# Performance work log

Hardware: AMD Instinct MI355X
Metric: run time of the kernel (lower is better)

Reference implementation:

```python
import jax, jax.numpy as jnp
import numpy as np

V, H, L, NH, MAXS = 32000, 1024, 6, 16, 2048
HD = H // NH
FF = 4 * H
EPS = 1e-5


def _ln(x, s, b):
    m = jnp.mean(x, axis=-1, keepdims=True)
    v = jnp.mean(jnp.square(x - m), axis=-1, keepdims=True)
    return (x - m) * jax.lax.rsqrt(v + EPS) * s + b


def setup_inputs() -> dict:
    key = jax.random.key(0)
    ks = jax.random.split(key, 12)
    s = 0.02
    inp = {
        "input_ids": jax.random.randint(ks[0], (2, 1024), 0, V, dtype=jnp.int64),
        "token_emb": jax.random.normal(ks[1], (V, H), jnp.float32) * s,
        "pos_emb": jax.random.normal(ks[2], (MAXS, H), jnp.float32) * s,
        "ln1_s": jnp.ones((L, H), jnp.float32),
        "ln1_b": jnp.zeros((L, H), jnp.float32),
        "qkv_w": jax.random.normal(ks[3], (L, H, 3 * H), jnp.float32) * s,
        "qkv_b": jnp.zeros((L, 3 * H), jnp.float32),
        "out_w": jax.random.normal(ks[4], (L, H, H), jnp.float32) * s,
        "out_b": jnp.zeros((L, H), jnp.float32),
        "ln2_s": jnp.ones((L, H), jnp.float32),
        "ln2_b": jnp.zeros((L, H), jnp.float32),
        "w1": jax.random.normal(ks[5], (L, H, FF), jnp.float32) * s,
        "b1": jnp.zeros((L, FF), jnp.float32),
        "w2": jax.random.normal(ks[6], (L, FF, H), jnp.float32) * s,
        "b2": jnp.zeros((L, H), jnp.float32),
        "lnf_s": jnp.ones((H,), jnp.float32),
        "lnf_b": jnp.zeros((H,), jnp.float32),
        "lm_w": jax.random.normal(ks[7], (H, V), jnp.float32) * s,
    }
    return inp


def reference(input_ids, token_emb, pos_emb, ln1_s, ln1_b, qkv_w, qkv_b,
              out_w, out_b, ln2_s, ln2_b, w1, b1, w2, b2, lnf_s, lnf_b, lm_w):
    B, S = input_ids.shape
    x = token_emb[input_ids] + pos_emb[:S][None]  # [B,S,H]; dropout = identity (eval)
    for i in range(L):
        # --- attention block ---
        h = _ln(x, ln1_s[i], ln1_b[i])
        qkv = h @ qkv_w[i] + qkv_b[i]                      # [B,S,3H]
        q, k, v = jnp.split(qkv, 3, axis=-1)
        q = q.reshape(B, S, NH, HD)
        k = k.reshape(B, S, NH, HD)
        v = v.reshape(B, S, NH, HD)
        scores = jnp.einsum('bqhd,bkhd->bhqk', q, k) / jnp.sqrt(jnp.float32(HD))
        attn = jax.nn.softmax(scores, axis=-1)             # non-causal, as in source
        o = jnp.einsum('bhqk,bkhd->bqhd', attn, v).reshape(B, S, H)
        x = x + o @ out_w[i] + out_b[i]
        # --- mlp block ---
        h = _ln(x, ln2_s[i], ln2_b[i])
        h = jax.nn.gelu(h @ w1[i] + b1[i], approximate=False)
        x = x + h @ w2[i] + b2[i]
    x = _ln(x, lnf_s, lnf_b)
    logits = x @ lm_w                                      # [B,S,V]
    return logits
```

## Files before the change

### kernel.cpp

```cpp
#include <hip/hip_runtime.h>
#include <hip/hip_bf16.h>
#include <cstdint>
#include <cstddef>

typedef __bf16 bf16;
typedef __attribute__((ext_vector_type(8))) __bf16 bf16x8;
typedef __attribute__((ext_vector_type(4))) __bf16 bf16x4;
typedef __attribute__((ext_vector_type(4))) float f32x4;

__device__ __forceinline__ f32x4 mfma16(bf16x8 a, bf16x8 b, f32x4 c) {
    return __builtin_amdgcn_mfma_f32_16x16x32_bf16(a, b, c, 0, 0, 0);
}

__device__ __forceinline__ void async_copy16(const void* g, void* l) {
    __builtin_amdgcn_global_load_lds((const __attribute__((address_space(1))) void*)g,
                                     (__attribute__((address_space(3))) void*)l,
                                     16, 0, 0);
}

template<int Ncnt> __device__ __forceinline__ void waitv();
template<> __device__ __forceinline__ void waitv<0>() { asm volatile("s_waitcnt vmcnt(0)" ::: "memory"); }
template<> __device__ __forceinline__ void waitv<2>() { asm volatile("s_waitcnt vmcnt(2)" ::: "memory"); }
template<> __device__ __forceinline__ void waitv<3>() { asm volatile("s_waitcnt vmcnt(3)" ::: "memory"); }
template<> __device__ __forceinline__ void waitv<4>() { asm volatile("s_waitcnt vmcnt(4)" ::: "memory"); }

__global__ __launch_bounds__(256)
void embed_kernel(const int* __restrict__ ids, const float* __restrict__ te,
                  const float* __restrict__ pe, float* __restrict__ x)
{
    const int row = blockIdx.x;
    const int s = row & 1023;
    const int id = ids[row];
    const f32x4* a = (const f32x4*)(te + (size_t)id * 1024);
    const f32x4* b = (const f32x4*)(pe + (size_t)s * 1024);
    f32x4* o = (f32x4*)(x + (size_t)row * 1024);
    o[threadIdx.x] = a[threadIdx.x] + b[threadIdx.x];
}

__device__ __forceinline__ void ln_body(const float* __restrict__ x, const float* __restrict__ sc,
                                        const float* __restrict__ bi, bf16* __restrict__ out,
                                        int row, int t, float* red)
{
    const f32x4 v = ((const f32x4*)(x + (size_t)row * 1024))[t];
    float s = v[0] + v[1] + v[2] + v[3];
    float q = v[0]*v[0] + v[1]*v[1] + v[2]*v[2] + v[3]*v[3];
    #pragma unroll
    for (int o = 1; o < 64; o <<= 1) { s += __shfl_xor(s, o); q += __shfl_xor(q, o); }
    const int wv = t >> 6, lane = t & 63;
    if (lane == 0) { red[wv] = s; red[4 + wv] = q; }
    __syncthreads();
    s = red[0] + red[1] + red[2] + red[3];
    q = red[4] + red[5] + red[6] + red[7];
    const float mean = s * (1.f / 1024.f);
    const float var  = q * (1.f / 1024.f) - mean * mean;
    const float rstd = rsqrtf(var + 1e-5f);
    const f32x4 scv = ((const f32x4*)sc)[t];
    const f32x4 biv = ((const f32x4*)bi)[t];
    bf16x4 o4;
    #pragma unroll
    for (int j = 0; j < 4; j++) o4[j] = (bf16)((v[j] - mean) * rstd * scv[j] + biv[j]);
    *(bf16x4*)(out + (size_t)row * 1024 + t * 4) = o4;
}

__device__ __forceinline__ void wcvt_body(const float* __restrict__ W, bf16* __restrict__ BT,
                                          int K, int N, int bid, int tidx, float (*tile)[65])
{
    const int nx = N >> 6;
    const int n0 = (bid % nx) << 6, k0 = (bid / nx) << 6;
    const int tx = tidx & 15, ty = tidx >> 4;
    #pragma unroll
    for (int r = 0; r < 4; r++) {
        const f32x4 v = *(const f32x4*)&W[(size_t)(k0 + ty + r*16) * N + n0 + tx*4];
        tile[ty + r*16][tx*4 + 0] = v[0];
        tile[ty + r*16][tx*4 + 1] = v[1];
        tile[ty + r*16][tx*4 + 2] = v[2];
        tile[ty + r*16][tx*4 + 3] = v[3];
    }
    __syncthreads();
    #pragma unroll
    for (int r = 0; r < 4; r++) {
        const int n = ty + r*16;
        bf16x4 o;
        #pragma unroll
        for (int j = 0; j < 4; j++) o[j] = (bf16)tile[tx*4 + j][n];
        *(bf16x4*)&BT[(size_t)(n0 + n) * K + k0 + tx*4] = o;
    }
}

__global__ __launch_bounds__(256)
void fused_ln_wcvt(const float* __restrict__ x, const float* __restrict__ sc,
                   const float* __restrict__ bi, bf16* __restrict__ out,
                   const float* __restrict__ W1, bf16* __restrict__ BT1, int K1, int N1, int nb1,
                   const float* __restrict__ W2, bf16* __restrict__ BT2, int K2, int N2)
{
    __shared__ float tile[64][65];
    __shared__ float red[8];
    const int bid = blockIdx.x, t = threadIdx.x;
    if (bid < 2048) {
        ln_body(x, sc, bi, out, bid, t, red);
    } else {
        const int wb = bid - 2048;
        if (wb < nb1) wcvt_body(W1, BT1, K1, N1, wb, t, tile);
        else          wcvt_body(W2, BT2, K2, N2, wb - nb1, t, tile);
    }
}

__global__ __launch_bounds__(256)
void fused_attn_wcvt(const bf16* __restrict__ qkv, bf16* __restrict__ attno,
                     const float* __restrict__ W, bf16* __restrict__ BT, int K, int N)
{
    __shared__ __align__(16) bf16 Ksh[128 * 64];
    __shared__ __align__(16) bf16 Vt[64][136];
    __shared__ __align__(16) bf16 Plds[4][16][132];
    __shared__ float tile[64][65];

    const int bid = blockIdx.x, tid = threadIdx.x;
    if (bid >= 512) {
        wcvt_body(W, BT, K, N, bid - 512, tid, tile);
        return;
    }
    const int b = (bid & 31) >> 4, h = bid & 15;
    const int qb = bid >> 5;
    const int lane = tid & 63, wave = tid >> 6;
    const bf16* base = qkv + (size_t)b * 1024 * 3072;
    const int qrow0 = qb * 64 + wave * 16;
    const int l15 = lane & 15;

    bf16x8 aQ[2];
    {
        const int qr = qrow0 + l15;
        const bf16* qp = base + (size_t)qr * 3072 + h * 64 + ((lane >> 4) << 3);
        aQ[0] = *(const bf16x8*)qp;
        aQ[1] = *(const bf16x8*)(qp + 32);
    }
    float m_i[4] = {-1e30f, -1e30f, -1e30f, -1e30f};
    float l_i[4] = {0.f, 0.f, 0.f, 0.f};
    f32x4 acc[4];
    #pragma unroll
    for (int nb = 0; nb < 4; nb++) acc[nb] = f32x4{0.f, 0.f, 0.f, 0.f};

    const int swzA = (((lane >> 4)     ^ (lane & 7)) << 3);
    const int swzB = (((4 + (lane >> 4)) ^ (lane & 7)) << 3);

    for (int ck = 0; ck < 8; ck++) {
        __syncthreads();
        #pragma unroll
        for (int p = 0; p < 4; p++) {
            const int c = p * 256 + tid;
            const int rw = c >> 3;
            const int kc = (c & 7) ^ (rw & 7);
            async_copy16(base + (size_t)(ck*128 + rw) * 3072 + 1024 + h*64 + kc*8, &Ksh[c * 8]);
        }
        #pragma unroll
        for (int p = 0; p < 4; p++) {
            const int idx = p * 256 + tid;
            const int keyl = idx >> 3, dc = idx & 7;
            const bf16x8 v = *(const bf16x8*)&base[(size_t)(ck*128 + keyl) * 3072 + 2048 + h*64 + dc*8];
            #pragma unroll
            for (int e = 0; e < 8; e++) Vt[dc*8 + e][keyl] = v[e];
        }
        __syncthreads();

        f32x4 sc[8];
        #pragma unroll
        for (int kk = 0; kk < 4; kk++) {
            const int kr0 = (kk*32 + l15) * 64;
            const int kr1 = kr0 + 16*64;
            f32x4 z{0.f, 0.f, 0.f, 0.f};
            z = mfma16(aQ[0], *(const bf16x8*)&Ksh[kr0 + swzA], z);
            z = mfma16(aQ[1], *(const bf16x8*)&Ksh[kr0 + swzB], z);
            sc[2*kk] = z;
            f32x4 z2{0.f, 0.f, 0.f, 0.f};
            z2 = mfma16(aQ[0], *(const bf16x8*)&Ksh[kr1 + swzA], z2);
            z2 = mfma16(aQ[1], *(const bf16x8*)&Ksh[kr1 + swzB], z2);
            sc[2*kk+1] = z2;
        }

        float c[4];
        #pragma unroll
        for (int i = 0; i < 4; i++) {
            float t = sc[0][i];
            #pragma unroll
            for (int e = 1; e < 8; e++) t = fmaxf(t, sc[e][i]);
            #pragma unroll
            for (int o = 1; o < 16; o <<= 1) t = fmaxf(t, __shfl_xor(t, o));
            t *= 0.125f;
            const float mnew = fmaxf(m_i[i], t);
            c[i] = __expf(m_i[i] - mnew);
            float p[8];
            float rs = 0.f;
            #pragma unroll
            for (int e = 0; e < 8; e++) {
                p[e] = __expf(fmaf(sc[e][i], 0.125f, -mnew));
                rs += p[e];
            }
            #pragma unroll
            for (int o = 1; o < 16; o <<= 1) rs += __shfl_xor(rs, o);
            l_i[i] = l_i[i] * c[i] + rs;
            m_i[i] = mnew;
            const int pr = ((lane >> 4) << 2) + i;
            #pragma unroll
            for (int e = 0; e < 8; e++)
                Plds[wave][pr][(e >> 1) * 32 + (e & 1) * 16 + l15] = (bf16)p[e];
        }
        #pragma unroll
        for (int nb = 0; nb < 4; nb++) {
            f32x4 a = acc[nb];
            a[0] *= c[0]; a[1] *= c[1]; a[2] *= c[2]; a[3] *= c[3];
            acc[nb] = a;
        }

        #pragma unroll
        for (int kk = 0; kk < 4; kk++) {
            const bf16x8 aP = *(const bf16x8*)&Plds[wave][l15][kk*32 + ((lane >> 4) << 3)];
            #pragma unroll
            for (int nb = 0; nb < 4; nb++) {
                const bf16x8 bV = *(const bf16x8*)&Vt[nb*16 + l15][kk*32 + ((lane >> 4) << 3)];
                acc[nb] = mfma16(aP, bV, acc[nb]);
            }
        }
    }
    #pragma unroll
    for (int nb = 0; nb < 4; nb++) {
        #pragma unroll
        for (int i = 0; i < 4; i++) {
            const int row = qrow0 + ((lane >> 4) << 2) + i;
            const float o = acc[nb][i] / l_i[i];
            attno[(size_t)(b*1024 + row) * 1024 + h*64 + nb*16 + l15] = (bf16)o;
        }
    }
}

template<int BM, int BN, int EPI, int KSPLIT>
__global__ __launch_bounds__(256)
void gemm_kernel(const bf16* __restrict__ A, const bf16* __restrict__ BT,
                 const float* __restrict__ bias, float* __restrict__ resid,
                 bf16* __restrict__ outb, float* __restrict__ outf,
                 int N, int K)
{
    constexpr int MT = 2048 / BM;
    constexpr int WM = BM / 2, WN = BN / 2;
    constexpr int FM = WM / 16, FN = WN / 16;
    constexpr int CA = BM / 32, CB = BN / 32;
    __shared__ __align__(16) bf16 Asmem[BM * 64];
    __shared__ __align__(16) bf16 Bsmem[BN * 64];

    const int nwg = gridDim.x;
    const int q = nwg >> 3, rr = nwg & 7;
    const int xcd = blockIdx.x & 7, ix = blockIdx.x >> 3;
    const int nid = (xcd < rr ? xcd * (q + 1) : rr * (q + 1) + (xcd - rr) * q) + ix;
    const int tiles = nwg / KSPLIT;
    const int ks = nid / tiles;
    const int tile = nid % tiles;
    const int bm = tile % MT, bn = tile / MT;

    const int tid = threadIdx.x;
    const int lane = tid & 63, wave = tid >> 6;
    const int wr = wave >> 1, wc = wave & 1;
    f32x4 acc[FM][FN];
    #pragma unroll
    for (int m = 0; m < FM; m++)
        #pragma unroll
        for (int n = 0; n < FN; n++) acc[m][n] = f32x4{0.f, 0.f, 0.f, 0.f};

    const bf16* Abase = A  + (size_t)bm * BM * K;
    const bf16* Bbase = BT + (size_t)bn * BN * K;
    const int K64 = K >> 6;
    const int ktlo = ks * (K64 / KSPLIT), kthi = ktlo + (K64 / KSPLIT);
    for (int kt = ktlo; kt < kthi; kt++) {
        __syncthreads();
        #pragma unroll
        for (int p = 0; p < CA; p++) {
            const int idx = p * 256 + tid;
            const int r = idx >> 3, c = (idx & 7) << 3;
            async_copy16(Abase + (size_t)r * K + kt * 64 + c, Asmem + idx * 8);
        }
        #pragma unroll
        for (int p = 0; p < CB; p++) {
            const int idx = p * 256 + tid;
            const int r = idx >> 3, c = (idx & 7) << 3;
            async_copy16(Bbase + (size_t)r * K + kt * 64 + c, Bsmem + idx * 8);
        }
        __syncthreads();
        #pragma unroll
        for (int kss = 0; kss < 2; kss++) {
            bf16x8 af[FM], bfv[FN];
            const int ko = kss * 32 + ((lane >> 4) << 3);
            const int ar = wr * WM + (lane & 15);
            const int br = wc * WN + (lane & 15);
            #pragma unroll
            for (int m = 0; m < FM; m++) af[m]  = *(const bf16x8*)&Asmem[(ar + m*16) * 64 + ko];
            #pragma unroll
            for (int n = 0; n < FN; n++) bfv[n] = *(const bf16x8*)&Bsmem[(br + n*16) * 64 + ko];
            #pragma unroll
            for (int m = 0; m < FM; m++)
                #pragma unroll
                for (int n = 0; n < FN; n++)
                    acc[m][n] = mfma16(af[m], bfv[n], acc[m][n]);
        }
    }
    const int r0 = bm * BM + wr * WM + ((lane >> 4) << 2);
    const int c0 = bn * BN + wc * WN + (lane & 15);
    #pragma unroll
    for (int n = 0; n < FN; n++) {
        const int col = c0 + n * 16;
        const float bv = (EPI == 3) ? 0.f : ((KSPLIT > 1 && ks != 0) ? 0.f : bias[col]);
        #pragma unroll
        for (int m = 0; m < FM; m++) {
            const int row = r0 + m * 16;
            const f32x4 a = acc[m][n];
            #pragma unroll
            for (int i = 0; i < 4; i++) {
                const float v = a[i] + bv;
                const size_t off = (size_t)(row + i) * N + col;
                if constexpr (EPI == 0) outb[off] = (bf16)v;
                else if constexpr (EPI == 1) {
                    if constexpr (KSPLIT > 1) atomicAdd(&resid[off], v);
                    else resid[off] += v;
                }
                else if constexpr (EPI == 2) {
                    const float g = 0.5f * v * (1.f + erff(v * 0.70710678118f));
                    outb[off] = (bf16)g;
                } else outf[off] = v;
            }
        }
    }
}

template<int BM, int BN, int EPI, int KSPLIT>
__global__ __launch_bounds__(512, 2)
void gemm256_kernel(const bf16* __restrict__ A, const bf16* __restrict__ BT,
                    const float* __restrict__ bias, float* __restrict__ resid,
                    bf16* __restrict__ outb, float* __restrict__ outf,
                    int N, int K)
{
    constexpr int MT = 2048 / BM;
    constexpr int FM = BM / 32;
    constexpr int FN = BN / 64;
    constexpr int HM = FM / 2;
    constexpr int LA = BM / 128, LB = BN / 128;
    constexpr int ASUB = BM * 32;
    constexpr int BSUB = BN * 32;
    extern __shared__ __align__(16) char smem_raw[];
    bf16* smem = (bf16*)smem_raw;

    const int nwg = gridDim.x;
    const int q = nwg >> 3, rr = nwg & 7;
    const int xcd = blockIdx.x & 7, ix = blockIdx.x >> 3;
    const int nid = (xcd < rr ? xcd * (q + 1) : rr * (q + 1) + (xcd - rr) * q) + ix;
    const int tiles = nwg / KSPLIT;
    const int ks = nid / tiles;
    const int tile = nid % tiles;
    const int bm = tile % MT, bn = tile / MT;

    const int tid = threadIdx.x, lane = tid & 63, wave = tid >> 6;
    const int wr = wave >> 2, wc = wave & 3;

    f32x4 acc[FM][FN];
    #pragma unroll
    for (int m = 0; m < FM; m++)
        #pragma unroll
        for (int n = 0; n < FN; n++) acc[m][n] = f32x4{0.f, 0.f, 0.f, 0.f};

    const bf16* Abase = A  + (size_t)bm * BM * K;
    const bf16* Bbase = BT + (size_t)bn * BN * K;
    const int Ts = (K >> 6) / KSPLIT;
    const int t0 = ks * Ts;

    const int l15 = lane & 15;
    const int swz = (((lane >> 4) ^ ((l15 >> 1) & 3)) << 3);
    const int arow0 = wr * (BM / 2) + l15;
    const int brow0 = wc * (BN / 4) + l15;

#define ABASE_(p_, ks_) (((p_)*2 + (ks_)) * ASUB)
#define BBASE_(p_, ks_) (4*ASUB + ((p_)*2 + (ks_)) * BSUB)
#define STAGE_A(p_, kt_, ks_) { _Pragma("unroll") for (int i = 0; i < LA; i++) { \
    const int c = tid + i * 512; const int rw = c >> 2; \
    const int kc = (c & 3) ^ ((rw >> 1) & 3); \
    async_copy16(Abase + (size_t)rw * K + (kt_)*64 + (ks_)*32 + kc*8, \
                 &smem[ABASE_(p_, ks_) + c*8]); } }
#define STAGE_B(p_, kt_, ks_) { _Pragma("unroll") for (int i = 0; i < LB; i++) { \
    const int c = tid + i * 512; const int rw = c >> 2; \
    const int kc = (c & 3) ^ ((rw >> 1) & 3); \
    async_copy16(Bbase + (size_t)rw * K + (kt_)*64 + (ks_)*32 + kc*8, \
                 &smem[BBASE_(p_, ks_) + c*8]); } }
#define LOAD_B(p_, ks_) { _Pragma("unroll") for (int n = 0; n < FN; n++) \
    bfv[n] = *(const bf16x8*)&smem[BBASE_(p_, ks_) + (brow0 + n*16)*32 + swz]; }
#define LOAD_A(p_, ks_, mg) { _Pragma("unroll") for (int m = 0; m < HM; m++) \
    af[m] = *(const bf16x8*)&smem[ABASE_(p_, ks_) + (arow0 + ((mg)*HM + m)*16)*32 + swz]; }
#define QUAD(mg) { __builtin_amdgcn_s_setprio(1); \
    _Pragma("unroll") for (int m = 0; m < HM; m++) \
      _Pragma("unroll") for (int n = 0; n < FN; n++) \
        acc[(mg)*HM + m][n] = mfma16(af[m], bfv[n], acc[(mg)*HM + m][n]); \
    __builtin_amdgcn_s_setprio(0); }

    STAGE_A(0, t0, 0); STAGE_B(0, t0, 0); STAGE_A(0, t0, 1); STAGE_B(0, t0, 1);
    waitv<LA + LB>();
    __builtin_amdgcn_s_barrier();

    for (int tl = 0; tl < Ts; tl++) {
        const int b = tl & 1;
        const int kt1 = t0 + tl + 1;
        const bool more = (tl + 1) < Ts;
        bf16x8 af[HM], bfv[FN];
        LOAD_B(b, 0); LOAD_A(b, 0, 0);
        if (more) STAGE_A(b ^ 1, kt1, 0);
        __builtin_amdgcn_s_barrier();
        QUAD(0);
        __builtin_amdgcn_s_barrier();
        LOAD_A(b, 0, 1);
        if (more) STAGE_B(b ^ 1, kt1, 0);
        __builtin_amdgcn_s_barrier();
        QUAD(1);
        if (more) waitv<LA + LB>(); else waitv<0>();
        __builtin_amdgcn_s_barrier();
        LOAD_B(b, 1); LOAD_A(b, 1, 0);
        if (more) STAGE_A(b ^ 1, kt1, 1);
        __builtin_amdgcn_s_barrier();
        QUAD(0);
        __builtin_amdgcn_s_barrier();
        LOAD_A(b, 1, 1);
        if (more) STAGE_B(b ^ 1, kt1, 1);
        __builtin_amdgcn_s_barrier();
        QUAD(1);
        if (more) waitv<LA + LB>();
        __builtin_amdgcn_s_barrier();
    }

    const int er = bm * BM + wr * (BM / 2) + ((lane >> 4) << 2);
    const int ec = bn * BN + wc * (BN / 4) + l15;
    #pragma unroll
    for (int n = 0; n < FN; n++) {
        const int col = ec + n * 16;
        const float bv = (EPI == 3) ? 0.f : ((KSPLIT > 1 && ks != 0) ? 0.f : bias[col]);
        #pragma unroll
        for (int m = 0; m < FM; m++) {
            #pragma unroll
            for (int i = 0; i < 4; i++) {
                const float v = acc[m][n][i] + bv;
                const size_t off = (size_t)(er + m * 16 + i) * N + col;
                if constexpr (EPI == 0) outb[off] = (bf16)v;
                else if constexpr (EPI == 1) {
                    if constexpr (KSPLIT > 1) atomicAdd(&resid[off], v);
                    else resid[off] += v;
                }
                else if constexpr (EPI == 2) {
                    outb[off] = (bf16)(0.5f * v * (1.f + erff(v * 0.70710678118f)));
                } else {
                    outf[off] = v;
                }
            }
        }
    }
#undef ABASE_
#undef BBASE_
#undef STAGE_A
#undef STAGE_B
#undef LOAD_A
#undef LOAD_B
#undef QUAD
}

extern "C" void kernel_launch(void* const* d_in, const int* in_sizes, int n_in,
                              void* d_out, int out_size, void* d_ws, size_t ws_size,
                              hipStream_t stream)
{
    const int*   ids     = (const int*)  d_in[0];
    const float* tok_emb = (const float*)d_in[1];
    const float* pos_emb = (const float*)d_in[2];
    const float* ln1_s   = (const float*)d_in[3];
    const float* ln1_b   = (const float*)d_in[4];
    const float* qkv_w   = (const float*)d_in[5];
    const float* qkv_b   = (const float*)d_in[6];
    const float* out_w   = (const float*)d_in[7];
    const float* out_b   = (const float*)d_in[8];
    const float* ln2_s   = (const float*)d_in[9];
    const float* ln2_b   = (const float*)d_in[10];
    const float* w1      = (const float*)d_in[11];
    const float* b1      = (const float*)d_in[12];
    const float* w2      = (const float*)d_in[13];
    const float* b2      = (const float*)d_in[14];
    const float* lnf_s   = (const float*)d_in[15];
    const float* lnf_b   = (const float*)d_in[16];
    const float* lm_w    = (const float*)d_in[17];

    char* ws = (char*)d_ws;
    float* x    = (float*)ws;  ws += (size_t)2048 * 1024 * 4;
    bf16*  h    = (bf16*)ws;   ws += (size_t)2048 * 1024 * 2;
    bf16*  qkvb = (bf16*)ws;   ws += (size_t)2048 * 3072 * 2;
    bf16*  attno= (bf16*)ws;   ws += (size_t)2048 * 1024 * 2;
    bf16*  ff   = (bf16*)ws;   ws += (size_t)2048 * 4096 * 2;
    bf16*  wTq  = (bf16*)ws;   ws += (size_t)3072 * 1024 * 2;
    bf16*  wTo  = (bf16*)ws;   ws += (size_t)1024 * 1024 * 2;
    bf16*  wT1  = (bf16*)ws;   ws += (size_t)4096 * 1024 * 2;
    bf16*  wT2  = (bf16*)ws;   ws += (size_t)1024 * 4096 * 2;
    bf16*  wTlm = (bf16*)ws;   ws += (size_t)32000 * 1024 * 2;

    embed_kernel<<<2048, 256, 0, stream>>>(ids, tok_emb, pos_emb, x);

    for (int l = 0; l < 6; l++) {
        if (l == 0) {
            fused_ln_wcvt<<<2048 + 768 + 8000, 256, 0, stream>>>(
                x, ln1_s, ln1_b, h,
                qkv_w, wTq, 1024, 3072, 768,
                lm_w, wTlm, 1024, 32000);
        } else {
            fused_ln_wcvt<<<2048 + 768, 256, 0, stream>>>(
                x, ln1_s + l*1024, ln1_b + l*1024, h,
                qkv_w + (size_t)l*1024*3072, wTq, 1024, 3072, 768,
                nullptr, nullptr, 0, 0);
        }
        gemm256_kernel<128,256,0,1><<<192, 512, 98304, stream>>>(h, wTq, qkv_b + l*3072, nullptr, qkvb, nullptr, 3072, 1024);
        fused_attn_wcvt<<<512 + 256, 256, 0, stream>>>(
            qkvb, attno, out_w + (size_t)l*1024*1024, wTo, 1024, 1024);
        gemm256_kernel<128,256,1,4><<<256, 512, 98304, stream>>>(attno, wTo, out_b + l*1024, x, nullptr, nullptr, 1024, 1024);
        fused_ln_wcvt<<<2048 + 1024 + 1024, 256, 0, stream>>>(
            x, ln2_s + l*1024, ln2_b + l*1024, h,
            w1 + (size_t)l*1024*4096, wT1, 1024, 4096, 1024,
            w2 + (size_t)l*4096*1024, wT2, 4096, 1024);
        gemm256_kernel<128,256,2,1><<<256, 512, 98304, stream>>>(h, wT1, b1 + l*4096, nullptr, ff, nullptr, 4096, 1024);
        gemm256_kernel<128,256,1,4><<<256, 512, 98304, stream>>>(ff, wT2, b2 + l*1024, x, nullptr, nullptr, 1024, 4096);
    }
    fused_ln_wcvt<<<2048, 256, 0, stream>>>(
        x, lnf_s, lnf_b, h,
        nullptr, nullptr, 0, 0, 0,
        nullptr, nullptr, 0, 0);
    gemm256_kernel<256,256,3,1><<<8*125, 512, 131072, stream>>>(h, wTlm, nullptr, nullptr, nullptr, (float*)d_out, 32000, 1024);
}
```

Before: 1.377 ms.

## Pre-transpose V into separate buffer and hoist out-proj weight conversion to front kernel

Measured after the change: 1.330 ms. 3.4% less time.

```diff
diff --git a/kernel.cpp b/kernel.cpp
--- a/kernel.cpp
+++ b/kernel.cpp
@@ -20,7 +20,6 @@
 
 template<int Ncnt> __device__ __forceinline__ void waitv();
 template<> __device__ __forceinline__ void waitv<0>() { asm volatile("s_waitcnt vmcnt(0)" ::: "memory"); }
-template<> __device__ __forceinline__ void waitv<2>() { asm volatile("s_waitcnt vmcnt(2)" ::: "memory"); }
 template<> __device__ __forceinline__ void waitv<3>() { asm volatile("s_waitcnt vmcnt(3)" ::: "memory"); }
 template<> __device__ __forceinline__ void waitv<4>() { asm volatile("s_waitcnt vmcnt(4)" ::: "memory"); }
 
@@ -88,6 +87,30 @@
 }
 
 __global__ __launch_bounds__(256)
+void front_kernel(const float* __restrict__ x, const float* __restrict__ sc,
+                  const float* __restrict__ bi, bf16* __restrict__ out,
+                  const float* __restrict__ qkvw0, bf16* __restrict__ wTq,
+                  const float* __restrict__ lmw, bf16* __restrict__ wTlm,
+                  const float* __restrict__ outw, bf16* __restrict__ wTo_all)
+{
+    __shared__ float tile[64][65];
+    __shared__ float red[8];
+    const int bid = blockIdx.x, t = threadIdx.x;
+    if (bid < 2048) {
+        ln_body(x, sc, bi, out, bid, t, red);
+    } else if (bid < 2048 + 768) {
+        wcvt_body(qkvw0, wTq, 1024, 3072, bid - 2048, t, tile);
+    } else if (bid < 2048 + 768 + 8000) {
+        wcvt_body(lmw, wTlm, 1024, 32000, bid - 2816, t, tile);
+    } else {
+        const int wb = bid - 10816;
+        const int l = wb >> 8;
+        wcvt_body(outw + (size_t)l * 1024 * 1024, wTo_all + (size_t)l * 1024 * 1024,
+                  1024, 1024, wb & 255, t, tile);
+    }
+}
+
+__global__ __launch_bounds__(256)
 void fused_ln_wcvt(const float* __restrict__ x, const float* __restrict__ sc,
                    const float* __restrict__ bi, bf16* __restrict__ out,
                    const float* __restrict__ W1, bf16* __restrict__ BT1, int K1, int N1, int nb1,
@@ -106,23 +129,46 @@
 }
 
 __global__ __launch_bounds__(256)
-void fused_attn_wcvt(const bf16* __restrict__ qkv, bf16* __restrict__ attno,
-                     const float* __restrict__ W, bf16* __restrict__ BT, int K, int N)
+void vtrans_kernel(const bf16* __restrict__ qkv, bf16* __restrict__ vT)
+{
+    __shared__ bf16 tile[128][72];
+    const int bh = blockIdx.x;
+    const int tt = blockIdx.y;
+    const int b = bh >> 4, h = bh & 15;
+    const bf16* src = qkv + (size_t)b * 1024 * 3072 + 2048 + h * 64;
+    const int tid = threadIdx.x;
+    #pragma unroll
+    for (int i = 0; i < 4; i++) {
+        const int c = i * 256 + tid;
+        const int tok = c >> 3, dc = c & 7;
+        *(bf16x8*)&tile[tok][dc * 8] = *(const bf16x8*)&src[(size_t)(tt*128 + tok) * 3072 + dc * 8];
+    }
+    __syncthreads();
+    #pragma unroll
+    for (int i = 0; i < 4; i++) {
+        const int c = i * 256 + tid;
+        const int d = c & 63, tc = c >> 6;
+        bf16x8 v;
+        #pragma unroll
+        for (int j = 0; j < 8; j++) v[j] = tile[tc*8 + j][d];
+        *(bf16x8*)&vT[((size_t)bh * 64 + d) * 1024 + tt*128 + tc*8] = v;
+    }
+}
+
+__global__ __launch_bounds__(256)
+void attn_kernel(const bf16* __restrict__ qkv, const bf16* __restrict__ vT,
+                 bf16* __restrict__ attno)
 {
     __shared__ __align__(16) bf16 Ksh[128 * 64];
-    __shared__ __align__(16) bf16 Vt[64][136];
+    __shared__ __align__(16) bf16 Vt[64 * 128];
     __shared__ __align__(16) bf16 Plds[4][16][132];
-    __shared__ float tile[64][65];
 
     const int bid = blockIdx.x, tid = threadIdx.x;
-    if (bid >= 512) {
-        wcvt_body(W, BT, K, N, bid - 512, tid, tile);
-        return;
-    }
     const int b = (bid & 31) >> 4, h = bid & 15;
     const int qb = bid >> 5;
     const int lane = tid & 63, wave = tid >> 6;
     const bf16* base = qkv + (size_t)b * 1024 * 3072;
+    const bf16* vbase = vT + (size_t)(b*16 + h) * 64 * 1024;
     const int qrow0 = qb * 64 + wave * 16;
     const int l15 = lane & 15;
 
@@ -153,11 +199,10 @@
         }
         #pragma unroll
         for (int p = 0; p < 4; p++) {
-            const int idx = p * 256 + tid;
-            const int keyl = idx >> 3, dc = idx & 7;
-            const bf16x8 v = *(const bf16x8*)&base[(size_t)(ck*128 + keyl) * 3072 + 2048 + h*64 + dc*8];
-            #pragma unroll
-            for (int e = 0; e < 8; e++) Vt[dc*8 + e][keyl] = v[e];
+            const int c = p * 256 + tid;
+            const int rw = c >> 4;
+            const int kc = (c & 15) ^ (rw & 7);
+            async_copy16(vbase + (size_t)rw * 1024 + ck*128 + kc*8, &Vt[c * 8]);
         }
         __syncthreads();
 
@@ -215,7 +260,9 @@
             const bf16x8 aP = *(const bf16x8*)&Plds[wave][l15][kk*32 + ((lane >> 4) << 3)];
             #pragma unroll
             for (int nb = 0; nb < 4; nb++) {
-                const bf16x8 bV = *(const bf16x8*)&Vt[nb*16 + l15][kk*32 + ((lane >> 4) << 3)];
+                const int r = nb*16 + l15;
+                const int chk = (kk*4 + (lane >> 4)) ^ (r & 7);
+                const bf16x8 bV = *(const bf16x8*)&Vt[r*128 + chk*8];
                 acc[nb] = mfma16(aP, bV, acc[nb]);
             }
         }
@@ -227,102 +274,6 @@
             const int row = qrow0 + ((lane >> 4) << 2) + i;
             const float o = acc[nb][i] / l_i[i];
             attno[(size_t)(b*1024 + row) * 1024 + h*64 + nb*16 + l15] = (bf16)o;
-        }
-    }
-}
-
-template<int BM, int BN, int EPI, int KSPLIT>
-__global__ __launch_bounds__(256)
-void gemm_kernel(const bf16* __restrict__ A, const bf16* __restrict__ BT,
-                 const float* __restrict__ bias, float* __restrict__ resid,
-                 bf16* __restrict__ outb, float* __restrict__ outf,
-                 int N, int K)
-{
-    constexpr int MT = 2048 / BM;
-    constexpr int WM = BM / 2, WN = BN / 2;
-    constexpr int FM = WM / 16, FN = WN / 16;
-    constexpr int CA = BM / 32, CB = BN / 32;
-    __shared__ __align__(16) bf16 Asmem[BM * 64];
-    __shared__ __align__(16) bf16 Bsmem[BN * 64];
-
-    const int nwg = gridDim.x;
-    const int q = nwg >> 3, rr = nwg & 7;
-    const int xcd = blockIdx.x & 7, ix = blockIdx.x >> 3;
-    const int nid = (xcd < rr ? xcd * (q + 1) : rr * (q + 1) + (xcd - rr) * q) + ix;
-    const int tiles = nwg / KSPLIT;
-    const int ks = nid / tiles;
-    const int tile = nid % tiles;
-    const int bm = tile % MT, bn = tile / MT;
-
-    const int tid = threadIdx.x;
-    const int lane = tid & 63, wave = tid >> 6;
-    const int wr = wave >> 1, wc = wave & 1;
-    f32x4 acc[FM][FN];
-    #pragma unroll
-    for (int m = 0; m < FM; m++)
-        #pragma unroll
-        for (int n = 0; n < FN; n++) acc[m][n] = f32x4{0.f, 0.f, 0.f, 0.f};
-
-    const bf16* Abase = A  + (size_t)bm * BM * K;
-    const bf16* Bbase = BT + (size_t)bn * BN * K;
-    const int K64 = K >> 6;
-    const int ktlo = ks * (K64 / KSPLIT), kthi = ktlo + (K64 / KSPLIT);
-    for (int kt = ktlo; kt < kthi; kt++) {
-        __syncthreads();
-        #pragma unroll
-        for (int p = 0; p < CA; p++) {
-            const int idx = p * 256 + tid;
-            const int r = idx >> 3, c = (idx & 7) << 3;
-            async_copy16(Abase + (size_t)r * K + kt * 64 + c, Asmem + idx * 8);
-        }
-        #pragma unroll
-        for (int p = 0; p < CB; p++) {
-            const int idx = p * 256 + tid;
-            const int r = idx >> 3, c = (idx & 7) << 3;
-            async_copy16(Bbase + (size_t)r * K + kt * 64 + c, Bsmem + idx * 8);
-        }
-        __syncthreads();
-        #pragma unroll
-        for (int kss = 0; kss < 2; kss++) {
-            bf16x8 af[FM], bfv[FN];
-            const int ko = kss * 32 + ((lane >> 4) << 3);
-            const int ar = wr * WM + (lane & 15);
-            const int br = wc * WN + (lane & 15);
-            #pragma unroll
-            for (int m = 0; m < FM; m++) af[m]  = *(const bf16x8*)&Asmem[(ar + m*16) * 64 + ko];
-            #pragma unroll
-            for (int n = 0; n < FN; n++) bfv[n] = *(const bf16x8*)&Bsmem[(br + n*16) * 64 + ko];
-            #pragma unroll
-            for (int m = 0; m < FM; m++)
-                #pragma unroll
-                for (int n = 0; n < FN; n++)
-                    acc[m][n] = mfma16(af[m], bfv[n], acc[m][n]);
-        }
-    }
-    const int r0 = bm * BM + wr * WM + ((lane >> 4) << 2);
-    const int c0 = bn * BN + wc * WN + (lane & 15);
-    #pragma unroll
-    for (int n = 0; n < FN; n++) {
-        const int col = c0 + n * 16;
-        const float bv = (EPI == 3) ? 0.f : ((KSPLIT > 1 && ks != 0) ? 0.f : bias[col]);
-        #pragma unroll
-        for (int m = 0; m < FM; m++) {
-            const int row = r0 + m * 16;
-            const f32x4 a = acc[m][n];
-            #pragma unroll
-            for (int i = 0; i < 4; i++) {
-                const float v = a[i] + bv;
-                const size_t off = (size_t)(row + i) * N + col;
-                if constexpr (EPI == 0) outb[off] = (bf16)v;
-                else if constexpr (EPI == 1) {
-                    if constexpr (KSPLIT > 1) atomicAdd(&resid[off], v);
-                    else resid[off] += v;
-                }
-                else if constexpr (EPI == 2) {
-                    const float g = 0.5f * v * (1.f + erff(v * 0.70710678118f));
-                    outb[off] = (bf16)g;
-                } else outf[off] = v;
-            }
         }
     }
 }
@@ -489,9 +440,10 @@
     bf16*  h    = (bf16*)ws;   ws += (size_t)2048 * 1024 * 2;
     bf16*  qkvb = (bf16*)ws;   ws += (size_t)2048 * 3072 * 2;
     bf16*  attno= (bf16*)ws;   ws += (size_t)2048 * 1024 * 2;
+    bf16*  vT   = (bf16*)ws;   ws += (size_t)32 * 64 * 1024 * 2;
     bf16*  ff   = (bf16*)ws;   ws += (size_t)2048 * 4096 * 2;
     bf16*  wTq  = (bf16*)ws;   ws += (size_t)3072 * 1024 * 2;
-    bf16*  wTo  = (bf16*)ws;   ws += (size_t)1024 * 1024 * 2;
+    bf16*  wTo_all = (bf16*)ws; ws += (size_t)6 * 1024 * 1024 * 2;
     bf16*  wT1  = (bf16*)ws;   ws += (size_t)4096 * 1024 * 2;
     bf16*  wT2  = (bf16*)ws;   ws += (size_t)1024 * 4096 * 2;
     bf16*  wTlm = (bf16*)ws;   ws += (size_t)32000 * 1024 * 2;
@@ -500,10 +452,9 @@
 
     for (int l = 0; l < 6; l++) {
         if (l == 0) {
-            fused_ln_wcvt<<<2048 + 768 + 8000, 256, 0, stream>>>(
+            front_kernel<<<12352, 256, 0, stream>>>(
                 x, ln1_s, ln1_b, h,
-                qkv_w, wTq, 1024, 3072, 768,
-                lm_w, wTlm, 1024, 32000);
+                qkv_w, wTq, lm_w, wTlm, out_w, wTo_all);
         } else {
             fused_ln_wcvt<<<2048 + 768, 256, 0, stream>>>(
                 x, ln1_s + l*1024, ln1_b + l*1024, h,
@@ -511,9 +462,9 @@
                 nullptr, nullptr, 0, 0);
         }
         gemm256_kernel<128,256,0,1><<<192, 512, 98304, stream>>>(h, wTq, qkv_b + l*3072, nullptr, qkvb, nullptr, 3072, 1024);
-        fused_attn_wcvt<<<512 + 256, 256, 0, stream>>>(
-            qkvb, attno, out_w + (size_t)l*1024*1024, wTo, 1024, 1024);
-        gemm256_kernel<128,256,1,4><<<256, 512, 98304, stream>>>(attno, wTo, out_b + l*1024, x, nullptr, nullptr, 1024, 1024);
+        vtrans_kernel<<<dim3(32, 8), 256, 0, stream>>>(qkvb, vT);
+        attn_kernel<<<512, 256, 0, stream>>>(qkvb, vT, attno);
+        gemm256_kernel<128,256,1,4><<<256, 512, 98304, stream>>>(attno, wTo_all + (size_t)l*1024*1024, out_b + l*1024, x, nullptr, nullptr, 1024, 1024);
         fused_ln_wcvt<<<2048 + 1024 + 1024, 256, 0, stream>>>(
             x, ln2_s + l*1024, ln2_b + l*1024, h,
             w1 + (size_t)l*1024*4096, wT1, 1024, 4096, 1024,
```
